# Kernel optimization log

Hardware: AMD Instinct MI355X
Metric: run time of the kernel (lower is better)

## Reference

```python
import jax, jax.numpy as jnp
import numpy as np

N_NODES = 20000
N_EDGES = 320000
IN_DIM = 256
HID = 128
HEADS = 4
NEG_SLOPE = 0.2


def _init_params(key):
    ks = jax.random.split(key, 16)
    s1 = 1.0 / np.sqrt(IN_DIM)
    s2 = 1.0 / np.sqrt(HID * HEADS)
    s3 = 1.0 / np.sqrt(HID)
    p = {
        # conv1: GATv2Conv(IN_DIM, HID, heads=HEADS, concat=True)
        'W1l': jax.random.normal(ks[0], (IN_DIM, HEADS * HID), jnp.float32) * s1,
        'b1l': jnp.zeros((HEADS * HID,), jnp.float32),
        'W1r': jax.random.normal(ks[1], (IN_DIM, HEADS * HID), jnp.float32) * s1,
        'b1r': jnp.zeros((HEADS * HID,), jnp.float32),
        'att1': jax.random.normal(ks[2], (HEADS, HID), jnp.float32) * s3,
        'bias1': jnp.zeros((HEADS * HID,), jnp.float32),
        # conv2: GATv2Conv(HID*HEADS, HID, heads=1, concat=False)
        'W2l': jax.random.normal(ks[3], (HID * HEADS, HID), jnp.float32) * s2,
        'b2l': jnp.zeros((HID,), jnp.float32),
        'W2r': jax.random.normal(ks[4], (HID * HEADS, HID), jnp.float32) * s2,
        'b2r': jnp.zeros((HID,), jnp.float32),
        'att2': jax.random.normal(ks[5], (1, HID), jnp.float32) * s3,
        'bias2': jnp.zeros((HID,), jnp.float32),
        # heads
        'Wa': jax.random.normal(ks[6], (HID, 1), jnp.float32) * s3,
        'ba': jnp.zeros((1,), jnp.float32),
        'Wrc': jax.random.normal(ks[7], (HID, 1), jnp.float32) * s3,
        'brc': jnp.zeros((1,), jnp.float32),
    }
    return p


def setup_inputs() -> dict:
    key = jax.random.key(0)
    kx, ke, kp = jax.random.split(key, 3)
    inp = {
        'x': jax.random.normal(kx, (N_NODES, IN_DIM), jnp.float32),
        'edge_index': jax.random.randint(ke, (2, N_EDGES), 0, N_NODES, jnp.int64),
    }
    inp.update(_init_params(kp))
    return inp


def _gatv2(x, Wl, bl, Wr, br, att, bias, src, dst, heads, out_ch, concat):
    # GATv2: e_ij = att . leaky_relu(lin_l(x_j) + lin_r(x_i)), softmax over dst,
    # out_i = sum_j alpha_ij * lin_l(x_j)
    n = x.shape[0]
    xl = (x @ Wl + bl).reshape(n, heads, out_ch)  # source transform
    xr = (x @ Wr + br).reshape(n, heads, out_ch)  # target transform
    e = jax.nn.leaky_relu(xl[src] + xr[dst], NEG_SLOPE)  # [E,H,C]
    score = jnp.einsum('ehc,hc->eh', e, att)              # [E,H]
    smax = jax.ops.segment_max(score, dst, num_segments=n)  # [N,H]
    ex = jnp.exp(score - smax[dst])
    denom = jax.ops.segment_sum(ex, dst, num_segments=n)
    alpha = ex / (denom[dst] + 1e-16)                     # [E,H]
    msg = alpha[..., None] * xl[src]                      # [E,H,C]
    out = jax.ops.segment_sum(msg, dst, num_segments=n)   # [N,H,C]
    if concat:
        out = out.reshape(n, heads * out_ch)
    else:
        out = out.mean(axis=1)
    return out + bias


def reference(x, edge_index, W1l, b1l, W1r, b1r, att1, bias1,
              W2l, b2l, W2r, b2r, att2, bias2, Wa, ba, Wrc, brc):
    src, dst = edge_index[0], edge_index[1]
    h = _gatv2(x, W1l, b1l, W1r, b1r, att1, bias1, src, dst, HEADS, HID, True)
    h = jax.nn.elu(h)
    # dropout p=0.2 is identity in eval mode
    h = _gatv2(h, W2l, b2l, W2r, b2r, att2, bias2, src, dst, 1, HID, False)
    anomaly = jax.nn.sigmoid(h @ Wa + ba)
    root_cause = jax.nn.sigmoid(h @ Wrc + brc)
    return anomaly, root_cause
```

## Files before the change

### kernel.cpp

```cpp
#include <hip/hip_runtime.h>
#include <hip/hip_bf16.h>

#define N_NODES 20000
#define N_EDGES 320000
#define IN_DIM 256
#define HID 128
#define HEADS 4
#define MPAD 20096

typedef unsigned short u16;
typedef __attribute__((ext_vector_type(8))) short bf16x8;
typedef __attribute__((ext_vector_type(4))) float f32x4;
typedef __attribute__((address_space(1))) void g_void;
typedef __attribute__((address_space(3))) void l_void;

__device__ __forceinline__ float asf(unsigned int u) {
    union { unsigned int i; float f; } c; c.i = u; return c.f;
}
__device__ __forceinline__ float bflo(unsigned int u) { return asf(u << 16); }
__device__ __forceinline__ float bfhi(unsigned int u) { return asf(u & 0xffff0000u); }
__device__ __forceinline__ u16 f2bf(float f) {
    union { float f; unsigned int i; } c; c.f = f;
    return (u16)((c.i + 0x7FFF + ((c.i >> 16) & 1)) >> 16);
}

__global__ void hist_kernel(const int* __restrict__ dst, int* __restrict__ deg, int E) {
    int i = blockIdx.x * blockDim.x + threadIdx.x;
    if (i < E) atomicAdd(&deg[dst[i]], 1);
}

__global__ __launch_bounds__(1024) void scan_kernel(
    const int* __restrict__ deg, int* __restrict__ row_start,
    int* __restrict__ cursor, int n) {
    __shared__ int partial[1024];
    int t = threadIdx.x;
    int chunk = (n + 1023) / 1024;
    int begin = t * chunk;
    int end = min(begin + chunk, n);
    int s = 0;
    for (int i = begin; i < end; ++i) s += deg[i];
    partial[t] = s;
    __syncthreads();
    for (int off = 1; off < 1024; off <<= 1) {
        int v = (t >= off) ? partial[t - off] : 0;
        __syncthreads();
        partial[t] += v;
        __syncthreads();
    }
    int run = (t == 0) ? 0 : partial[t - 1];
    for (int i = begin; i < end; ++i) {
        row_start[i] = run;
        cursor[i] = run;
        run += deg[i];
    }
    if (t == 1023) row_start[n] = run;
}

__global__ void scatter_kernel(const int* __restrict__ dst, int* __restrict__ cursor,
                               int* __restrict__ seid, int* __restrict__ sdst, int E) {
    int i = blockIdx.x * blockDim.x + threadIdx.x;
    if (i < E) {
        int d = dst[i];
        int pos = atomicAdd(&cursor[d], 1);
        seid[pos] = i;
        sdst[pos] = d;
    }
}

__global__ void rank_kernel(const int* __restrict__ row_start, const int* __restrict__ seid,
                            const int* __restrict__ sdst, const int* __restrict__ src,
                            int* __restrict__ ssrc, int E) {
    int i = blockIdx.x * blockDim.x + threadIdx.x;
    if (i >= E) return;
    int d = sdst[i];
    int beg = row_start[d], end = row_start[d + 1];
    int my = seid[i];
    int rank = 0;
    for (int j = beg; j < end; ++j) rank += (seid[j] < my) ? 1 : 0;
    ssrc[beg + rank] = src[my];
}

__global__ void cast_x_kernel(const float* __restrict__ x, u16* __restrict__ xb) {
    int i = blockIdx.x * blockDim.x + threadIdx.x;
    const int nq = MPAD * IN_DIM / 4;
    if (i >= nq) return;
    int elem = i * 4;
    uint2 u;
    if (elem < N_NODES * IN_DIM) {
        float4 v = ((const float4*)x)[i];
        u.x = (unsigned)f2bf(v.x) | ((unsigned)f2bf(v.y) << 16);
        u.y = (unsigned)f2bf(v.z) | ((unsigned)f2bf(v.w) << 16);
    } else {
        u.x = 0u; u.y = 0u;
    }
    *(uint2*)(xb + elem) = u;
}

__global__ __launch_bounds__(256) void transpose_all_kernel(
    const float* __restrict__ W1l, const float* __restrict__ W1r,
    const float* __restrict__ W2l, const float* __restrict__ W2r,
    u16* __restrict__ BT1, u16* __restrict__ BT2) {
    const float* W; u16* out; int K, N;
    switch (blockIdx.z) {
        case 0:  W = W1l; out = BT1;             K = 256; N = 512; break;
        case 1:  W = W1r; out = BT1 + 512 * 256; K = 256; N = 512; break;
        case 2:  W = W2l; out = BT2;             K = 512; N = 128; break;
        default: W = W2r; out = BT2 + 128 * 512; K = 512; N = 128; break;
    }
    int bx = blockIdx.x * 32;
    int by = blockIdx.y * 32;
    if (bx >= N || by >= K) return;
    __shared__ float t[32][33];
    int tx = threadIdx.x, ty = threadIdx.y;
    #pragma unroll
    for (int j = 0; j < 32; j += 8)
        t[ty + j][tx] = W[(size_t)(by + ty + j) * N + bx + tx];
    __syncthreads();
    #pragma unroll
    for (int j = 0; j < 32; j += 8)
        out[(size_t)(bx + ty + j) * K + by + tx] = f2bf(t[tx][ty + j]);
}

__global__ void prep_bias_kernel(const float* b1l, const float* b1r,
                                 const float* b2l, const float* b2r,
                                 float* bc1, float* bc2) {
    int t = threadIdx.x;
    if (t < 512) bc1[t] = b1l[t];
    else bc1[t] = b1r[t - 512];
    if (t < 128) bc2[t] = b2l[t];
    else if (t < 256) bc2[t] = b2r[t - 128];
}

__global__ __launch_bounds__(256) void gemm_bf16_kernel(
    const u16* __restrict__ A, const u16* __restrict__ BT,
    const float* __restrict__ bias, u16* __restrict__ C,
    int K, int Mrows, int N) {
    __shared__ u16 As[4096];
    __shared__ u16 Bs[4096];
    const int tid = threadIdx.x;
    const int lane = tid & 63;
    const int wid = tid >> 6;
    const int wr = wid >> 1, wc = wid & 1;
    const int brow = blockIdx.y * 128, bcol = blockIdx.x * 128;

    const int srow = tid >> 2;
    const int skk = (((tid & 3) ^ ((tid >> 3) & 3))) * 8;
    const u16* ga0 = A + (size_t)(brow + srow) * K + skk;
    const u16* ga1 = A + (size_t)(brow + 64 + srow) * K + skk;
    const u16* gb0 = BT + (size_t)(bcol + srow) * K + skk;
    const u16* gb1 = BT + (size_t)(bcol + 64 + srow) * K + skk;
    u16* lA0 = As + tid * 8;
    u16* lA1 = As + 2048 + tid * 8;
    u16* lB0 = Bs + tid * 8;
    u16* lB1 = Bs + 2048 + tid * 8;

    const int fr = lane & 15;
    const int fg = lane >> 4;
    const int fslot = (fg ^ ((fr >> 1) & 3)) * 8;
    const u16* ra = As + (wr * 64 + fr) * 32 + fslot;
    const u16* rb = Bs + (wc * 64 + fr) * 32 + fslot;

    f32x4 acc[4][4];
    #pragma unroll
    for (int m = 0; m < 4; ++m)
        #pragma unroll
        for (int n = 0; n < 4; ++n)
            acc[m][n] = (f32x4){0.f, 0.f, 0.f, 0.f};

    for (int k0 = 0; k0 < K; k0 += 32) {
        __builtin_amdgcn_global_load_lds((const g_void*)(ga0 + k0), (l_void*)lA0, 16, 0, 0);
        __builtin_amdgcn_global_load_lds((const g_void*)(ga1 + k0), (l_void*)lA1, 16, 0, 0);
        __builtin_amdgcn_global_load_lds((const g_void*)(gb0 + k0), (l_void*)lB0, 16, 0, 0);
        __builtin_amdgcn_global_load_lds((const g_void*)(gb1 + k0), (l_void*)lB1, 16, 0, 0);
        __syncthreads();
        bf16x8 av[4], bv[4];
        #pragma unroll
        for (int m = 0; m < 4; ++m) av[m] = *(const bf16x8*)(ra + m * 512);
        #pragma unroll
        for (int n = 0; n < 4; ++n) bv[n] = *(const bf16x8*)(rb + n * 512);
        #pragma unroll
        for (int m = 0; m < 4; ++m)
            #pragma unroll
            for (int n = 0; n < 4; ++n)
                acc[m][n] = __builtin_amdgcn_mfma_f32_16x16x32_bf16(av[m], bv[n], acc[m][n], 0, 0, 0);
        __syncthreads();
    }

    const int col0 = bcol + wc * 64 + fr;
    const int row0 = brow + wr * 64 + fg * 4;
    #pragma unroll
    for (int n = 0; n < 4; ++n) {
        const int col = col0 + n * 16;
        const float bv2 = bias[col];
        #pragma unroll
        for (int m = 0; m < 4; ++m) {
            const int r0 = row0 + m * 16;
            #pragma unroll
            for (int j = 0; j < 4; ++j) {
                int r = r0 + j;
                if (r < Mrows) C[(size_t)r * N + col] = f2bf(acc[m][n][j] + bv2);
            }
        }
    }
}

#define UNPACK8(c, f) \
    f[0] = bflo(c.x); f[1] = bfhi(c.x); f[2] = bflo(c.y); f[3] = bfhi(c.y); \
    f[4] = bflo(c.z); f[5] = bfhi(c.z); f[6] = bflo(c.w); f[7] = bfhi(c.w);

__global__ __launch_bounds__(256) void fused1_kernel(
    const u16* __restrict__ xlr, const int* __restrict__ row_start,
    const int* __restrict__ ssrc, const float* __restrict__ att1,
    const float* __restrict__ bias1, u16* __restrict__ h1, int n) {
    int node = blockIdx.x * 4 + (threadIdx.x >> 6);
    int lane = threadIdx.x & 63;
    if (node >= n) return;

    uint4 xr4 = *(const uint4*)(xlr + (size_t)node * 1024 + 512 + lane * 8);
    float xrf[8];
    UNPACK8(xr4, xrf);
    float4 w0 = ((const float4*)att1)[lane * 2];
    float4 w1 = ((const float4*)att1)[lane * 2 + 1];
    float wa[8] = {w0.x, w0.y, w0.z, w0.w, w1.x, w1.y, w1.z, w1.w};

    int beg = row_start[node], end = row_start[node + 1];
    float l = 0.f;
    float acc[8] = {0.f, 0.f, 0.f, 0.f, 0.f, 0.f, 0.f, 0.f};

    uint4 v0 = {0, 0, 0, 0}, v1 = {0, 0, 0, 0};
    if (beg < end)     v0 = *(const uint4*)(xlr + (size_t)ssrc[beg] * 1024 + lane * 8);
    if (beg + 1 < end) v1 = *(const uint4*)(xlr + (size_t)ssrc[beg + 1] * 1024 + lane * 8);

    for (int p = beg; p < end; p += 2) {
        uint4 c0 = v0, c1 = v1;
        if (p + 2 < end) v0 = *(const uint4*)(xlr + (size_t)ssrc[p + 2] * 1024 + lane * 8);
        if (p + 3 < end) v1 = *(const uint4*)(xlr + (size_t)ssrc[p + 3] * 1024 + lane * 8);

        float xf[8];
        UNPACK8(c0, xf);
        float sc = 0.f;
        #pragma unroll
        for (int j = 0; j < 8; ++j) {
            float v = xf[j] + xrf[j];
            sc = fmaf(fmaxf(v, 0.2f * v), wa[j], sc);
        }
        sc += __shfl_xor(sc, 1);
        sc += __shfl_xor(sc, 2);
        sc += __shfl_xor(sc, 4);
        sc += __shfl_xor(sc, 8);
        float pv = __expf(sc);
        l += pv;
        #pragma unroll
        for (int j = 0; j < 8; ++j) acc[j] = fmaf(pv, xf[j], acc[j]);

        if (p + 1 < end) {
            float yf[8];
            UNPACK8(c1, yf);
            float sc1 = 0.f;
            #pragma unroll
            for (int j = 0; j < 8; ++j) {
                float v = yf[j] + xrf[j];
                sc1 = fmaf(fmaxf(v, 0.2f * v), wa[j], sc1);
            }
            sc1 += __shfl_xor(sc1, 1);
            sc1 += __shfl_xor(sc1, 2);
            sc1 += __shfl_xor(sc1, 4);
            sc1 += __shfl_xor(sc1, 8);
            float pv1 = __expf(sc1);
            l += pv1;
            #pragma unroll
            for (int j = 0; j < 8; ++j) acc[j] = fmaf(pv1, yf[j], acc[j]);
        }
    }

    float inv = 1.f / (l + 1e-16f);
    float4 b0 = ((const float4*)bias1)[lane * 2];
    float4 b1 = ((const float4*)bias1)[lane * 2 + 1];
    float bb[8] = {b0.x, b0.y, b0.z, b0.w, b1.x, b1.y, b1.z, b1.w};
    bf16x8 outv;
    #pragma unroll
    for (int j = 0; j < 8; ++j) {
        float v = fmaf(acc[j], inv, bb[j]);
        v = v > 0.f ? v : __expf(v) - 1.f;
        outv[j] = (short)f2bf(v);
    }
    *(bf16x8*)(h1 + (size_t)node * 512 + lane * 8) = outv;
}

__global__ __launch_bounds__(256) void fused2_kernel(
    const u16* __restrict__ xlr2, const int* __restrict__ row_start,
    const int* __restrict__ ssrc, const float* __restrict__ att2,
    const float* __restrict__ bias2, const float* __restrict__ Wa,
    const float* __restrict__ ba, const float* __restrict__ Wrc,
    const float* __restrict__ brc, float* __restrict__ out, int n) {
    int node = blockIdx.x * 4 + (threadIdx.x >> 6);
    int lane = threadIdx.x & 63;
    if (node >= n) return;

    unsigned int xr = *(const unsigned int*)(xlr2 + (size_t)node * 256 + 128 + lane * 2);
    float xr0 = bflo(xr), xr1 = bfhi(xr);
    float2 w = ((const float2*)att2)[lane];

    int beg = row_start[node], end = row_start[node + 1];
    float l = 0.f, acc0 = 0.f, acc1 = 0.f;

    unsigned int v0 = 0, v1 = 0;
    if (beg < end)     v0 = *(const unsigned int*)(xlr2 + (size_t)ssrc[beg] * 256 + lane * 2);
    if (beg + 1 < end) v1 = *(const unsigned int*)(xlr2 + (size_t)ssrc[beg + 1] * 256 + lane * 2);

    for (int p = beg; p < end; p += 2) {
        unsigned int c0 = v0, c1 = v1;
        if (p + 2 < end) v0 = *(const unsigned int*)(xlr2 + (size_t)ssrc[p + 2] * 256 + lane * 2);
        if (p + 3 < end) v1 = *(const unsigned int*)(xlr2 + (size_t)ssrc[p + 3] * 256 + lane * 2);

        float x0 = bflo(c0), x1 = bfhi(c0);
        float t0 = x0 + xr0, t1 = x1 + xr1;
        float sc = fmaxf(t0, 0.2f * t0) * w.x + fmaxf(t1, 0.2f * t1) * w.y;
        #pragma unroll
        for (int off = 1; off < 64; off <<= 1) sc += __shfl_xor(sc, off);
        float pv = __expf(sc);
        l += pv;
        acc0 = fmaf(pv, x0, acc0);
        acc1 = fmaf(pv, x1, acc1);

        if (p + 1 < end) {
            float y0 = bflo(c1), y1 = bfhi(c1);
            float u0 = y0 + xr0, u1 = y1 + xr1;
            float sc1 = fmaxf(u0, 0.2f * u0) * w.x + fmaxf(u1, 0.2f * u1) * w.y;
            #pragma unroll
            for (int off = 1; off < 64; off <<= 1) sc1 += __shfl_xor(sc1, off);
            float pv1 = __expf(sc1);
            l += pv1;
            acc0 = fmaf(pv1, y0, acc0);
            acc1 = fmaf(pv1, y1, acc1);
        }
    }

    float inv = 1.f / (l + 1e-16f);
    int c0i = lane * 2, c1i = lane * 2 + 1;
    float h0 = fmaf(acc0, inv, bias2[c0i]);
    float h1v = fmaf(acc1, inv, bias2[c1i]);
    float a = h0 * Wa[c0i] + h1v * Wa[c1i];
    float r = h0 * Wrc[c0i] + h1v * Wrc[c1i];
    #pragma unroll
    for (int off = 1; off < 64; off <<= 1) {
        a += __shfl_xor(a, off);
        r += __shfl_xor(r, off);
    }
    if (lane == 0) {
        out[node]     = 1.f / (1.f + __expf(-(a + ba[0])));
        out[n + node] = 1.f / (1.f + __expf(-(r + brc[0])));
    }
}

extern "C" void kernel_launch(void* const* d_in, const int* in_sizes, int n_in,
                              void* d_out, int out_size, void* d_ws, size_t ws_size,
                              hipStream_t stream) {
    const float* x    = (const float*)d_in[0];
    const int* ei     = (const int*)d_in[1];
    const float* W1l  = (const float*)d_in[2];
    const float* b1l  = (const float*)d_in[3];
    const float* W1r  = (const float*)d_in[4];
    const float* b1r  = (const float*)d_in[5];
    const float* att1 = (const float*)d_in[6];
    const float* bias1= (const float*)d_in[7];
    const float* W2l  = (const float*)d_in[8];
    const float* b2l  = (const float*)d_in[9];
    const float* W2r  = (const float*)d_in[10];
    const float* b2r  = (const float*)d_in[11];
    const float* att2 = (const float*)d_in[12];
    const float* bias2= (const float*)d_in[13];
    const float* Wa   = (const float*)d_in[14];
    const float* ba   = (const float*)d_in[15];
    const float* Wrc  = (const float*)d_in[16];
    const float* brc  = (const float*)d_in[17];
    float* out = (float*)d_out;

    const int N = N_NODES, E = N_EDGES;
    const int* src = ei;
    const int* dst = ei + E;

    char* ws = (char*)d_ws;
    u16*   xlr1 = (u16*)ws;
    u16*   h1b  = (u16*)(ws + 41156608);
    u16*   xb   = (u16*)(ws + 61734912);
    u16*   xlr2 = (u16*)(ws + 61734912);
    u16*   BT1  = (u16*)(ws + 72024064);
    u16*   BT2  = (u16*)(ws + 72548352);
    float* bc1  = (float*)(ws + 72810496);
    float* bc2  = (float*)(ws + 72814592);
    int* deg       = (int*)(ws + 72815616);
    int* row_start = (int*)(ws + 72896000);
    int* cursor    = (int*)(ws + 72976128);
    int* ssrc      = (int*)(ws + 73056128);
    int* seid      = (int*)(ws + 74336128);
    int* sdst      = (int*)(ws + 75616128);

    hipMemsetAsync(deg, 0, N * sizeof(int), stream);
    hist_kernel<<<(E + 255) / 256, 256, 0, stream>>>(dst, deg, E);
    scan_kernel<<<1, 1024, 0, stream>>>(deg, row_start, cursor, N);
    scatter_kernel<<<(E + 255) / 256, 256, 0, stream>>>(dst, cursor, seid, sdst, E);
    rank_kernel<<<(E + 255) / 256, 256, 0, stream>>>(row_start, seid, sdst, src, ssrc, E);

    cast_x_kernel<<<(MPAD * IN_DIM / 4 + 255) / 256, 256, 0, stream>>>(x, xb);
    transpose_all_kernel<<<dim3(16, 16, 4), dim3(32, 8), 0, stream>>>(
        W1l, W1r, W2l, W2r, BT1, BT2);
    prep_bias_kernel<<<1, 1024, 0, stream>>>(b1l, b1r, b2l, b2r, bc1, bc2);

    gemm_bf16_kernel<<<dim3(8, 157), 256, 0, stream>>>(xb, BT1, bc1, xlr1, 256, N, 1024);
    fused1_kernel<<<(N + 3) / 4, 256, 0, stream>>>(xlr1, row_start, ssrc, att1, bias1, h1b, N);

    gemm_bf16_kernel<<<dim3(2, 157), 256, 0, stream>>>(h1b, BT2, bc2, xlr2, 512, N, 256);
    fused2_kernel<<<(N + 3) / 4, 256, 0, stream>>>(xlr2, row_start, ssrc, att2, bias2,
                                                   Wa, ba, Wrc, brc, out, N);
}
```

Before: 251.0 us.

## Stage GEMM epilogue through LDS for vector stores and swizzle blocks across XCDs

```diff
diff --git a/kernel.cpp b/kernel.cpp
--- a/kernel.cpp
+++ b/kernel.cpp
@@ -22,6 +22,11 @@
 __device__ __forceinline__ u16 f2bf(float f) {
     union { float f; unsigned int i; } c; c.f = f;
     return (u16)((c.i + 0x7FFF + ((c.i >> 16) & 1)) >> 16);
+}
+__device__ __forceinline__ int xcd_swz(int orig, int nwg) {
+    int q = nwg >> 3, r = nwg & 7;
+    int xcd = orig & 7, lin = orig >> 3;
+    return (xcd < r ? xcd * (q + 1) : r * (q + 1) + (xcd - r) * q) + lin;
 }
 
 __global__ void hist_kernel(const int* __restrict__ dst, int* __restrict__ deg, int E) {
@@ -134,14 +139,16 @@
 __global__ __launch_bounds__(256) void gemm_bf16_kernel(
     const u16* __restrict__ A, const u16* __restrict__ BT,
     const float* __restrict__ bias, u16* __restrict__ C,
-    int K, int Mrows, int N) {
-    __shared__ u16 As[4096];
-    __shared__ u16 Bs[4096];
+    int K, int N, int nbx) {
+    __shared__ u16 smem[8192];
+    u16* As = smem;
+    u16* Bs = smem + 4096;
     const int tid = threadIdx.x;
     const int lane = tid & 63;
     const int wid = tid >> 6;
     const int wr = wid >> 1, wc = wid & 1;
-    const int brow = blockIdx.y * 128, bcol = blockIdx.x * 128;
+    const int wg = xcd_swz(blockIdx.x, gridDim.x);
+    const int brow = (wg / nbx) * 128, bcol = (wg % nbx) * 128;
 
     const int srow = tid >> 2;
     const int skk = (((tid & 3) ^ ((tid >> 3) & 3))) * 8;
@@ -186,20 +193,33 @@
         __syncthreads();
     }
 
-    const int col0 = bcol + wc * 64 + fr;
-    const int row0 = brow + wr * 64 + fg * 4;
-    #pragma unroll
-    for (int n = 0; n < 4; ++n) {
-        const int col = col0 + n * 16;
-        const float bv2 = bias[col];
-        #pragma unroll
-        for (int m = 0; m < 4; ++m) {
-            const int r0 = row0 + m * 16;
+    float bv4[4];
+    #pragma unroll
+    for (int n = 0; n < 4; ++n) bv4[n] = bias[bcol + wc * 64 + n * 16 + fr];
+    #pragma unroll
+    for (int ph = 0; ph < 2; ++ph) {
+        __syncthreads();
+        if (wr == ph) {
             #pragma unroll
-            for (int j = 0; j < 4; ++j) {
-                int r = r0 + j;
-                if (r < Mrows) C[(size_t)r * N + col] = f2bf(acc[m][n][j] + bv2);
-            }
+            for (int m = 0; m < 4; ++m)
+                #pragma unroll
+                for (int n = 0; n < 4; ++n) {
+                    const int cc = wc * 64 + n * 16 + fr;
+                    #pragma unroll
+                    for (int j = 0; j < 4; ++j) {
+                        const int rr = m * 16 + fg * 4 + j;
+                        smem[rr * 128 + (cc ^ (((rr >> 2) & 3) << 4))] =
+                            f2bf(acc[m][n][j] + bv4[n]);
+                    }
+                }
+        }
+        __syncthreads();
+        #pragma unroll
+        for (int it = 0; it < 4; ++it) {
+            const int rr = it * 16 + (tid >> 4);
+            const int cc0 = (tid & 15) * 8;
+            *(bf16x8*)(C + (size_t)(brow + ph * 64 + rr) * N + bcol + cc0) =
+                *(const bf16x8*)(smem + rr * 128 + (cc0 ^ (((rr >> 2) & 3) << 4)));
         }
     }
 }
@@ -407,10 +427,10 @@
         W1l, W1r, W2l, W2r, BT1, BT2);
     prep_bias_kernel<<<1, 1024, 0, stream>>>(b1l, b1r, b2l, b2r, bc1, bc2);
 
-    gemm_bf16_kernel<<<dim3(8, 157), 256, 0, stream>>>(xb, BT1, bc1, xlr1, 256, N, 1024);
+    gemm_bf16_kernel<<<157 * 8, 256, 0, stream>>>(xb, BT1, bc1, xlr1, 256, 1024, 8);
     fused1_kernel<<<(N + 3) / 4, 256, 0, stream>>>(xlr1, row_start, ssrc, att1, bias1, h1b, N);
 
-    gemm_bf16_kernel<<<dim3(2, 157), 256, 0, stream>>>(h1b, BT2, bc2, xlr2, 512, N, 256);
+    gemm_bf16_kernel<<<157 * 2, 256, 0, stream>>>(h1b, BT2, bc2, xlr2, 512, 256, 2);
     fused2_kernel<<<(N + 3) / 4, 256, 0, stream>>>(xlr2, row_start, ssrc, att2, bias2,
                                                    Wa, ba, Wrc, brc, out, N);
 }
```

Result: faster. 227.7 us (-9.3%).
